# Kernel tuning notes

Measured on AMD Instinct MI355X. Metric: run time of the kernel, lower is better.

## Reference

```python
import jax, jax.numpy as jnp
import numpy as np

CHANNELS = 256
DIM = 256          # next power of two of CHANNELS (equal here, so no padding)
STAGES = 8         # log2(DIM)
TOTAL_PAIRS = STAGES * (DIM // 2)  # 1024
CAP = 0.99
B, H, W = 32, 64, 64


def setup_inputs() -> dict:
    key = jax.random.key(0)
    ks = jax.random.split(key, 6)
    return {
        "x": jax.random.normal(ks[0], (B, CHANNELS, H, W), dtype=jnp.float32),
        "modulation": jax.random.normal(ks[1], (B, CHANNELS), dtype=jnp.float32),
        "angles": jax.random.normal(ks[2], (TOTAL_PAIRS,), dtype=jnp.float32) * 0.1,
        "diagonal": jax.random.normal(ks[3], (DIM,), dtype=jnp.float32) * 0.1,
        "w_angle": jax.random.normal(ks[4], (TOTAL_PAIRS, CHANNELS), dtype=jnp.float32) * 0.02,
        "w_diag": jax.random.normal(ks[5], (DIM, CHANNELS), dtype=jnp.float32) * 0.02,
    }


def _apply_stage(y, stage_angles, block):
    # y: (b, DIM, h, w); stage_angles: (b, DIM//2)
    half = block // 2
    b, _, h, w = y.shape
    y = y.reshape(b, DIM // block, block, h, w)
    ang = stage_angles.reshape(b, DIM // block, half)[..., None, None]  # (b, nb, half, 1, 1)
    c, s = jnp.cos(ang), jnp.sin(ang)
    left = y[:, :, :half]
    right = y[:, :, half:]
    new_left = c * left + s * right
    new_right = -s * left + c * right
    return jnp.concatenate([new_left, new_right], axis=2).reshape(b, DIM, h, w)


def reference(x, modulation, angles, diagonal, w_angle, w_diag):
    # channels == DIM (power of two) -> padding is a no-op
    batch = x.shape[0]
    base_angles = angles[None, :]                                   # (1, TOTAL_PAIRS)
    base_diag = jnp.clip(jnp.tanh(diagonal), -CAP, CAP)[None, :]    # (1, DIM)

    angle_delta = jnp.tanh(modulation @ w_angle.T)                  # (b, TOTAL_PAIRS)
    diag_delta = jnp.tanh(modulation @ w_diag.T)                    # (b, DIM)
    all_angles = base_angles + angle_delta
    diag = base_diag + diag_delta

    y = x
    per_stage = DIM // 2
    offset = 0
    for stage in range(STAGES):
        block = 2 ** (stage + 1)
        stage_angles = all_angles[:, offset:offset + per_stage]
        y = _apply_stage(y, stage_angles, block)
        offset += per_stage

    diag = jnp.clip(diag.reshape(batch, DIM), -CAP, CAP)
    y = y * diag[:, :, None, None]
    return y
```

## Files before the change

kernel.cpp:

```cpp
#include <hip/hip_runtime.h>
#include <math.h>

#define CAPV 0.99f

#define WG_BARRIER() do {                                   \
    asm volatile("s_waitcnt lgkmcnt(0)" ::: "memory");      \
    __builtin_amdgcn_s_barrier();                           \
    asm volatile("" ::: "memory");                          \
} while (0)

__global__ void pr_precompute(const float* __restrict__ mod,
                              const float* __restrict__ angles,
                              const float* __restrict__ diagonal,
                              const float* __restrict__ w_angle,
                              const float* __restrict__ w_diag,
                              float2* __restrict__ cs,
                              float* __restrict__ diag2) {
    const int gid = blockIdx.x * blockDim.x + threadIdx.x;
    const int o = gid >> 2;
    const int r = gid & 3;

    if (o < 32768) {
        const int b = o >> 10;
        const int p = o & 1023;
        const float4* m = (const float4*)(mod + (size_t)b * 256);
        const float4* w = (const float4*)(w_angle + (size_t)p * 256);
        float acc = 0.f;
#pragma unroll
        for (int i = 0; i < 16; ++i) {
            const float4 a = m[i * 4 + r];
            const float4 c = w[i * 4 + r];
            acc += a.x * c.x + a.y * c.y + a.z * c.z + a.w * c.w;
        }
        acc += __shfl_xor(acc, 1, 64);
        acc += __shfl_xor(acc, 2, 64);
        if (r == 0) {
            const float ang = angles[p] + tanhf(acc);
            float sv, cv;
            sincosf(ang, &sv, &cv);
            int outp;
            if (p < 512) {
                outp = p;
            } else {
                const int st   = (p >> 7) + 1;
                const int lp   = p & 127;
                const int half = 1 << (st - 1);
                const int c    = ((lp >> (st - 1)) << st) | (lp & (half - 1));
                const int k    = c >> 4;
                const int c0   = c & 15;
                int q;
                if (st == 5)      q = k >> 1;
                else if (st == 6) q = (k >> 2) * 2 + (k & 1);
                else if (st == 7) q = (k >> 3) * 4 + (k & 3);
                else              q = k;
                outp = 512 + (st - 5) * 128 + c0 * 8 + q;
            }
            cs[(size_t)b * 1024 + outp] = make_float2(cv, sv);
        }
    } else {
        const int o2 = o - 32768;
        const int b2 = o2 >> 8;
        const int cd = o2 & 255;
        const float4* m = (const float4*)(mod + (size_t)b2 * 256);
        const float4* w = (const float4*)(w_diag + (size_t)cd * 256);
        float acc = 0.f;
#pragma unroll
        for (int i = 0; i < 16; ++i) {
            const float4 a = m[i * 4 + r];
            const float4 c = w[i * 4 + r];
            acc += a.x * c.x + a.y * c.y + a.z * c.z + a.w * c.w;
        }
        acc += __shfl_xor(acc, 1, 64);
        acc += __shfl_xor(acc, 2, 64);
        if (r == 0) {
            float bd = tanhf(diagonal[cd]);
            bd = fminf(fmaxf(bd, -CAPV), CAPV);
            float d = bd + tanhf(acc);
            d = fminf(fmaxf(d, -CAPV), CAPV);
            diag2[(size_t)b2 * 256 + (cd & 15) * 16 + (cd >> 4)] = d;
        }
    }
}

__global__ __launch_bounds__(512, 4)
void pr_butterfly(const float* __restrict__ x,
                  const float2* __restrict__ cs,
                  const float* __restrict__ diag2,
                  float* __restrict__ out) {
    __shared__ __align__(16) float tile[256 * 64];

    const int tid  = threadIdx.x;
    const int blk  = blockIdx.x;
    const int widx = blk & 63;
    const int bg   = blk >> 6;

    const int lane = tid & 63;
    const int wv   = tid >> 6;
    const int rr   = tid >> 4;
    const int sl   = tid & 15;
    const int A    = lane >> 2;
    const int pq   = lane & 3;
    const int p    = wv * 8 + pq * 2;
    const int pl   = p & 3;
    const int ps   = p >> 2;

    const int ptB = widx * 64;

    float4 rfA[8], rfB[8];

    {
        const float* xb0 = x + (size_t)(bg * 4) * 1048576;
        const float* xb1 = xb0 + 1048576;
#pragma unroll
        for (int it = 0; it < 8; ++it) {
            const int row = it * 32 + rr;
            rfA[it] = *(const float4*)(xb0 + (size_t)row * 4096 + ptB + sl * 4);
        }
#pragma unroll
        for (int it = 0; it < 8; ++it) {
            const int row = it * 32 + rr;
            rfB[it] = *(const float4*)(xb1 + (size_t)row * 4096 + ptB + sl * 4);
        }
    }

#pragma unroll
    for (int t = 0; t < 4; ++t) {
        const int b = bg * 4 + t;
        float* __restrict__ ob = out + (size_t)b * 1048576;
        const float2* __restrict__ csb = cs + (size_t)b * 1024;

#pragma unroll
        for (int it = 0; it < 8; ++it) {
            const int row = it * 32 + rr;
            const int swz = ((row ^ (row >> 4)) & 3) << 1;
            const float4 v = (t & 1) ? rfB[it] : rfA[it];
            *(float4*)&tile[row * 64 + ((sl ^ swz) << 2)] = v;
        }

        if (t < 2) {
            const float* xbn = x + (size_t)(b + 2) * 1048576;
#pragma unroll
            for (int it = 0; it < 8; ++it) {
                const int row = it * 32 + rr;
                const float4 v = *(const float4*)(xbn + (size_t)row * 4096 + ptB + sl * 4);
                if (t & 1) rfB[it] = v; else rfA[it] = v;
            }
        }

        WG_BARRIER();

        {
            float2 y[16];
#pragma unroll
            for (int j = 0; j < 16; ++j) {
                const int swz = ((j ^ A) & 3) << 1;
                y[j] = *(const float2*)&tile[(A * 16 + j) * 64 + ((ps ^ swz) << 2) + pl];
            }

#pragma unroll
            for (int st = 1; st <= 4; ++st) {
                const int h = 1 << (st - 1);
                const float4* c4 = (const float4*)(csb + ((st - 1) * 128 + A * 8));
                float4 cq[4];
#pragma unroll
                for (int i = 0; i < 4; ++i) cq[i] = c4[i];
#pragma unroll
                for (int q = 0; q < 8; ++q) {
                    const int jl = ((q >> (st - 1)) << st) | (q & (h - 1));
                    const int jr = jl | h;
                    const float cc = (q & 1) ? cq[q >> 1].z : cq[q >> 1].x;
                    const float ss = (q & 1) ? cq[q >> 1].w : cq[q >> 1].y;
                    const float2 l = y[jl];
                    const float2 r = y[jr];
                    y[jl].x = fmaf(cc, l.x, ss * r.x);
                    y[jl].y = fmaf(cc, l.y, ss * r.y);
                    y[jr].x = fmaf(cc, r.x, -(ss * l.x));
                    y[jr].y = fmaf(cc, r.y, -(ss * l.y));
                }
            }

#pragma unroll
            for (int j = 0; j < 16; ++j) {
                const int swz = ((j ^ A) & 3) << 1;
                *(float2*)&tile[(A * 16 + j) * 64 + ((ps ^ swz) << 2) + pl] = y[j];
            }
        }

        asm volatile("s_waitcnt lgkmcnt(0)" ::: "memory");

        {
            float2 z[16];
#pragma unroll
            for (int k = 0; k < 16; ++k) {
                const int swz = ((A ^ k) & 3) << 1;
                z[k] = *(const float2*)&tile[(A + k * 16) * 64 + ((ps ^ swz) << 2) + pl];
            }

#pragma unroll
            for (int st = 5; st <= 8; ++st) {
                const int sb = st - 5;
                const float4* c4 = (const float4*)csb + 256 + sb * 64 + A * 4;
                float4 cq[4];
#pragma unroll
                for (int i = 0; i < 4; ++i) cq[i] = c4[i];
#pragma unroll
                for (int q = 0; q < 8; ++q) {
                    int k;
                    if (st == 5)      k = q * 2;
                    else if (st == 6) k = (q >> 1) * 4 + (q & 1);
                    else if (st == 7) k = (q >> 2) * 8 + (q & 3);
                    else              k = q;
                    const int k2 = k + (1 << sb);
                    const float cc = (q & 1) ? cq[q >> 1].z : cq[q >> 1].x;
                    const float ss = (q & 1) ? cq[q >> 1].w : cq[q >> 1].y;
                    const float2 l = z[k];
                    const float2 r = z[k2];
                    z[k].x  = fmaf(cc, l.x, ss * r.x);
                    z[k].y  = fmaf(cc, l.y, ss * r.y);
                    z[k2].x = fmaf(cc, r.x, -(ss * l.x));
                    z[k2].y = fmaf(cc, r.y, -(ss * l.y));
                }
            }

            {
                const float4* d4 = (const float4*)(diag2 + (size_t)b * 256 + A * 16);
#pragma unroll
                for (int i = 0; i < 4; ++i) {
                    const float4 dv = d4[i];
                    z[i * 4 + 0].x *= dv.x;  z[i * 4 + 0].y *= dv.x;
                    z[i * 4 + 1].x *= dv.y;  z[i * 4 + 1].y *= dv.y;
                    z[i * 4 + 2].x *= dv.z;  z[i * 4 + 2].y *= dv.z;
                    z[i * 4 + 3].x *= dv.w;  z[i * 4 + 3].y *= dv.w;
                }
            }

#pragma unroll
            for (int k = 0; k < 16; ++k) {
                const int swz = ((A ^ k) & 3) << 1;
                *(float2*)&tile[(A + k * 16) * 64 + ((ps ^ swz) << 2) + pl] = z[k];
            }
        }

        WG_BARRIER();

#pragma unroll
        for (int it = 0; it < 8; ++it) {
            const int row = it * 32 + rr;
            const int swz = ((row ^ (row >> 4)) & 3) << 1;
            const float4 v = *(const float4*)&tile[row * 64 + ((sl ^ swz) << 2)];
            *(float4*)(ob + (size_t)row * 4096 + ptB + sl * 4) = v;
        }
    }
}

extern "C" void kernel_launch(void* const* d_in, const int* in_sizes, int n_in,
                              void* d_out, int out_size, void* d_ws, size_t ws_size,
                              hipStream_t stream) {
    const float* x        = (const float*)d_in[0];
    const float* mod      = (const float*)d_in[1];
    const float* angles   = (const float*)d_in[2];
    const float* diagonal = (const float*)d_in[3];
    const float* w_angle  = (const float*)d_in[4];
    const float* w_diag   = (const float*)d_in[5];
    float* out = (float*)d_out;

    float2* cs    = (float2*)d_ws;
    float*  diag2 = (float*)((char*)d_ws + 32 * 1024 * sizeof(float2));

    pr_precompute<<<640, 256, 0, stream>>>(mod, angles, diagonal, w_angle, w_diag, cs, diag2);
    pr_butterfly<<<512, 512, 0, stream>>>(x, cs, diag2, out);
}
```

Before: 83.90 us.

## Halve butterfly tile width to 32 pixels, doubling workgroups

Shrinks the per-workgroup spatial tile from 64 to 32 pixels, so each thread handles one pixel column instead of two. LDS use halves and register arrays shrink, which allows a launch bound of 8 waves per SIMD and twice as many workgroups for more occupancy and latency hiding. The cost is that each workgroup reloads the cos/sin coefficients and diagonal for half as much data, and global accesses become 128-byte row segments instead of 256-byte ones. The swizzle patterns are adjusted to suit the narrower tile.

```diff
diff --git a/kernel.cpp b/kernel.cpp
--- a/kernel.cpp
+++ b/kernel.cpp
@@ -82,43 +82,41 @@
     }
 }
 
-__global__ __launch_bounds__(512, 4)
+__global__ __launch_bounds__(512, 8)
 void pr_butterfly(const float* __restrict__ x,
                   const float2* __restrict__ cs,
                   const float* __restrict__ diag2,
                   float* __restrict__ out) {
-    __shared__ __align__(16) float tile[256 * 64];
+    __shared__ __align__(16) float tile[256 * 32];
 
     const int tid  = threadIdx.x;
     const int blk  = blockIdx.x;
-    const int widx = blk & 63;
-    const int bg   = blk >> 6;
+    const int widx = blk & 127;
+    const int bg   = blk >> 7;
 
     const int lane = tid & 63;
     const int wv   = tid >> 6;
-    const int rr   = tid >> 4;
-    const int sl   = tid & 15;
+    const int rr   = tid >> 3;
+    const int sl   = tid & 7;
     const int A    = lane >> 2;
     const int pq   = lane & 3;
-    const int p    = wv * 8 + pq * 2;
-    const int pl   = p & 3;
-    const int ps   = p >> 2;
-
-    const int ptB = widx * 64;
-
-    float4 rfA[8], rfB[8];
+    const int p    = wv * 4 + pq;
+
+    const int ptB = widx * 32;
+
+    float4 rfA[4], rfB[4];
 
     {
         const float* xb0 = x + (size_t)(bg * 4) * 1048576;
         const float* xb1 = xb0 + 1048576;
 #pragma unroll
-        for (int it = 0; it < 8; ++it) {
-            const int row = it * 32 + rr;
+        for (int it = 0; it < 4; ++it) {
+            const int row = it * 64 + rr;
             rfA[it] = *(const float4*)(xb0 + (size_t)row * 4096 + ptB + sl * 4);
         }
 #pragma unroll
-        for (int it = 0; it < 8; ++it) {
-            const int row = it * 32 + rr;
+        for (int it = 0; it < 4; ++it) {
+            const int row = it * 64 + rr;
             rfB[it] = *(const float4*)(xb1 + (size_t)row * 4096 + ptB + sl * 4);
         }
     }
@@ -130,18 +128,18 @@
         const float2* __restrict__ csb = cs + (size_t)b * 1024;
 
 #pragma unroll
-        for (int it = 0; it < 8; ++it) {
-            const int row = it * 32 + rr;
-            const int swz = ((row ^ (row >> 4)) & 3) << 1;
+        for (int it = 0; it < 4; ++it) {
+            const int row = it * 64 + rr;
+            const int swz = (row ^ (row >> 4)) & 3;
             const float4 v = (t & 1) ? rfB[it] : rfA[it];
-            *(float4*)&tile[row * 64 + ((sl ^ swz) << 2)] = v;
+            *(float4*)&tile[row * 32 + ((sl ^ swz) << 2)] = v;
         }
 
         if (t < 2) {
             const float* xbn = x + (size_t)(b + 2) * 1048576;
 #pragma unroll
-            for (int it = 0; it < 8; ++it) {
-                const int row = it * 32 + rr;
+            for (int it = 0; it < 4; ++it) {
+                const int row = it * 64 + rr;
                 const float4 v = *(const float4*)(xbn + (size_t)row * 4096 + ptB + sl * 4);
                 if (t & 1) rfB[it] = v; else rfA[it] = v;
             }
@@ -150,11 +148,11 @@
         WG_BARRIER();
 
         {
-            float2 y[16];
+            float y[16];
 #pragma unroll
             for (int j = 0; j < 16; ++j) {
-                const int swz = ((j ^ A) & 3) << 1;
-                y[j] = *(const float2*)&tile[(A * 16 + j) * 64 + ((ps ^ swz) << 2) + pl];
+                const int swz = ((j ^ A) & 3) << 2;
+                y[j] = tile[(A * 16 + j) * 32 + (p ^ swz)];
             }
 
 #pragma unroll
@@ -170,30 +168,28 @@
                     const int jr = jl | h;
                     const float cc = (q & 1) ? cq[q >> 1].z : cq[q >> 1].x;
                     const float ss = (q & 1) ? cq[q >> 1].w : cq[q >> 1].y;
-                    const float2 l = y[jl];
-                    const float2 r = y[jr];
-                    y[jl].x = fmaf(cc, l.x, ss * r.x);
-                    y[jl].y = fmaf(cc, l.y, ss * r.y);
-                    y[jr].x = fmaf(cc, r.x, -(ss * l.x));
-                    y[jr].y = fmaf(cc, r.y, -(ss * l.y));
+                    const float l = y[jl];
+                    const float r = y[jr];
+                    y[jl] = fmaf(cc, l, ss * r);
+                    y[jr] = fmaf(cc, r, -(ss * l));
                 }
             }
 
 #pragma unroll
             for (int j = 0; j < 16; ++j) {
-                const int swz = ((j ^ A) & 3) << 1;
-                *(float2*)&tile[(A * 16 + j) * 64 + ((ps ^ swz) << 2) + pl] = y[j];
+                const int swz = ((j ^ A) & 3) << 2;
+                tile[(A * 16 + j) * 32 + (p ^ swz)] = y[j];
             }
         }
 
         asm volatile("s_waitcnt lgkmcnt(0)" ::: "memory");
 
         {
-            float2 z[16];
+            float z[16];
 #pragma unroll
             for (int k = 0; k < 16; ++k) {
-                const int swz = ((A ^ k) & 3) << 1;
-                z[k] = *(const float2*)&tile[(A + k * 16) * 64 + ((ps ^ swz) << 2) + pl];
+                const int swz = ((A ^ k) & 3) << 2;
+                z[k] = tile[(A + k * 16) * 32 + (p ^ swz)];
             }
 
 #pragma unroll
@@ -213,12 +209,10 @@
                     const int k2 = k + (1 << sb);
                     const float cc = (q & 1) ? cq[q >> 1].z : cq[q >> 1].x;
                     const float ss = (q & 1) ? cq[q >> 1].w : cq[q >> 1].y;
-                    const float2 l = z[k];
-                    const float2 r = z[k2];
-                    z[k].x  = fmaf(cc, l.x, ss * r.x);
-                    z[k].y  = fmaf(cc, l.y, ss * r.y);
-                    z[k2].x = fmaf(cc, r.x, -(ss * l.x));
-                    z[k2].y = fmaf(cc, r.y, -(ss * l.y));
+                    const float l = z[k];
+                    const float r = z[k2];
+                    z[k]  = fmaf(cc, l, ss * r);
+                    z[k2] = fmaf(cc, r, -(ss * l));
                 }
             }
 
@@ -227,27 +221,27 @@
 #pragma unroll
                 for (int i = 0; i < 4; ++i) {
                     const float4 dv = d4[i];
-                    z[i * 4 + 0].x *= dv.x;  z[i * 4 + 0].y *= dv.x;
-                    z[i * 4 + 1].x *= dv.y;  z[i * 4 + 1].y *= dv.y;
-                    z[i * 4 + 2].x *= dv.z;  z[i * 4 + 2].y *= dv.z;
-                    z[i * 4 + 3].x *= dv.w;  z[i * 4 + 3].y *= dv.w;
+                    z[i * 4 + 0] *= dv.x;
+                    z[i * 4 + 1] *= dv.y;
+                    z[i * 4 + 2] *= dv.z;
+                    z[i * 4 + 3] *= dv.w;
                 }
             }
 
 #pragma unroll
             for (int k = 0; k < 16; ++k) {
-                const int swz = ((A ^ k) & 3) << 1;
-                *(float2*)&tile[(A + k * 16) * 64 + ((ps ^ swz) << 2) + pl] = z[k];
+                const int swz = ((A ^ k) & 3) << 2;
+                tile[(A + k * 16) * 32 + (p ^ swz)] = z[k];
             }
         }
 
         WG_BARRIER();
 
 #pragma unroll
-        for (int it = 0; it < 8; ++it) {
-            const int row = it * 32 + rr;
-            const int swz = ((row ^ (row >> 4)) & 3) << 1;
-            const float4 v = *(const float4*)&tile[row * 64 + ((sl ^ swz) << 2)];
+        for (int it = 0; it < 4; ++it) {
+            const int row = it * 64 + rr;
+            const int swz = (row ^ (row >> 4)) & 3;
+            const float4 v = *(const float4*)&tile[row * 32 + ((sl ^ swz) << 2)];
             *(float4*)(ob + (size_t)row * 4096 + ptB + sl * 4) = v;
         }
     }
@@ -268,5 +262,5 @@
     float*  diag2 = (float*)((char*)d_ws + 32 * 1024 * sizeof(float2));
 
     pr_precompute<<<640, 256, 0, stream>>>(mod, angles, diagonal, w_angle, w_diag, cs, diag2);
-    pr_butterfly<<<512, 512, 0, stream>>>(x, cs, diag2, out);
+    pr_butterfly<<<1024, 512, 0, stream>>>(x, cs, diag2, out);
 }
```

Measured after the change: 111.7 us. 33.1% more time.
